# Kernel tuning notes

Measured on AMD Instinct MI355X. Metric: run time of the kernel, lower is better.

Reference implementation:

```python
import jax, jax.numpy as jnp
import numpy as np
import math

SIZE = (60, 270, 480)           # full video T, H, W
CHANNELS = 14                   # sum of per-level grid channels 8+4+2
GRID_SIZES = [(60, 16, 16, 8), (30, 8, 8, 4), (15, 4, 4, 2)]
IDX_MAX = (60, 3, 5)            # patch grid -> patch_size (1, 90, 96)
PADDING = (0, 1, 1)
N_PATCH = 64
MANIP_LBASE = 2.0
MANIP_LEVELS = 8
INIT_SCALE = 1e-3


def setup_inputs() -> dict:
    key = jax.random.key(0)
    kt, kh, kw = jax.random.split(key, 3)
    idx = jnp.stack([
        jax.random.randint(kt, (N_PATCH,), 0, IDX_MAX[0]),
        jax.random.randint(kh, (N_PATCH,), 0, IDX_MAX[1]),
        jax.random.randint(kw, (N_PATCH,), 0, IDX_MAX[2]),
    ], axis=1).astype(jnp.int32)
    inp = {
        "idx": idx,
        "idx_max": jnp.asarray(IDX_MAX, dtype=jnp.int32),
        "padding": jnp.asarray(PADDING, dtype=jnp.int32),
    }
    for i, (T, H, W, C) in enumerate(GRID_SIZES):
        k = jax.random.fold_in(key, 10 + i)
        inp[f"grid{i}"] = jax.random.normal(k, (T * H * W, C), jnp.float32) * INIT_SCALE
    return inp


def _pixel_idx_1d(ix, size_d, nmax_d, pad_d):
    # ix: [N] patch index along one dim -> ([N, P+2*pad] clipped pixel idx, mask)
    p = size_d // nmax_d
    offs = jnp.arange(-pad_d, p + pad_d)
    raw = ix[:, None] * p + offs[None, :]
    mask = ((raw >= 0) & (raw < size_d)).astype(jnp.float32)
    return jnp.clip(raw, 0, size_d - 1), mask


def reference(idx, idx_max, padding, grid0, grid1, grid2):
    T, H, W = SIZE
    im = tuple(int(v) for v in np.asarray(idx_max))
    pad = tuple(int(v) for v in np.asarray(padding))
    patch = tuple(SIZE[d] // im[d] for d in range(3))
    ppad = tuple(patch[d] + 2 * pad[d] for d in range(3))

    # Multi-level grids -> trilinear upsample to full (T,H,W,C_i), concat on C.
    # jax.image.resize 'trilinear' uses half-pixel centers == torch align_corners=False.
    enc_splits = []
    for g, (Tg, Hg, Wg, Cg) in zip((grid0, grid1, grid2), GRID_SIZES):
        enc_splits.append(jax.image.resize(g.reshape(Tg, Hg, Wg, Cg), (T, H, W, Cg), method="trilinear"))
    enc = jnp.concatenate(enc_splits, axis=-1).reshape(T * H * W, CHANNELS)

    it, mt = _pixel_idx_1d(idx[:, 0], T, im[0], pad[0])
    ih, mh = _pixel_idx_1d(idx[:, 1], H, im[1], pad[1])
    iw, mw = _pixel_idx_1d(idx[:, 2], W, im[2], pad[2])

    flat = (it[:, :, None, None] * (H * W) + ih[:, None, :, None] * W + iw[:, None, None, :]).reshape(-1)
    mask = (mt[:, :, None, None] * mh[:, None, :, None] * mw[:, None, None, :]).reshape(-1, 1)

    t_embed = (mask * enc[flat]).reshape((idx.shape[0],) + ppad + (CHANNELS,))

    bases = (MANIP_LBASE ** jnp.arange(MANIP_LEVELS, dtype=jnp.float32)) * math.pi
    v = idx[:, 0].astype(jnp.float32)[:, None] * bases
    t_manip = jnp.concatenate([jnp.sin(v), jnp.cos(v)], axis=-1)  # [N, 2*levels]

    return t_embed, t_manip
```

## Files before the change

kernel.cpp:

```cpp
#include <hip/hip_runtime.h>
#include <math.h>


#define N_PATCH 64
#define PPAD_H 92
#define PPAD_W 98
#define CH 14
#define PIX_PER_PATCH (PPAD_H * PPAD_W)
#define ROWS_PER_BLOCK 2
#define BLOCKS_PER_PATCH 46
#define PX_PER_BLOCK 196
#define F4_PER_BLOCK (PX_PER_BLOCK * CH / 4)
#define ELEMS_PER_PATCH (PIX_PER_PATCH * CH)
#define ELEMS_PER_BLOCK (PX_PER_BLOCK * CH)
#define TOTAL_EMBED (N_PATCH * ELEMS_PER_PATCH)
#define TOTAL_MANIP (N_PATCH * 16)

#define RB_STRIDE 72
#define L1_OFF 48
#define L2_OFF 64
#define BD_L1 40
#define BD_L2 52
#define BD_COUNT 56
#define BD_STRIDE 64

#define SW0 ((float)((double)16 / 480.0))
#define SW1 ((float)((double)8  / 480.0))
#define SW2 ((float)((double)4  / 480.0))
#define SH0 ((float)((double)16 / 270.0))
#define SH1 ((float)((double)8  / 270.0))
#define SH2 ((float)((double)4  / 270.0))

__device__ __forceinline__ float lerpf(float a, float b, float f) {
    return a + f * (b - a);
}

__device__ __forceinline__ int wcell0u(int rw0, float sw) {
    float x = ((float)rw0 + 0.5f) * sw - 0.5f;
    return (int)floorf(x);
}

__global__ __launch_bounds__(256) void embed_kernel(
    const int* __restrict__ idx,
    const float* __restrict__ g0,
    const float* __restrict__ g1,
    const float* __restrict__ g2,
    float* __restrict__ out)
{
    __shared__ __align__(16) float s_V[ROWS_PER_BLOCK][RB_STRIDE];
    __shared__ __align__(16) float s_B[ROWS_PER_BLOCK][BD_STRIDE];
    __shared__ __align__(16) float s_D[ROWS_PER_BLOCK][BD_STRIDE];
    __shared__ __align__(16) float s_buf[PX_PER_BLOCK * CH];

    const int tid = threadIdx.x;
    const int bx  = blockIdx.x;
    const int n   = blockIdx.y;
    const int it  = idx[3 * n + 0];
    const int ih  = idx[3 * n + 1];
    const int iw  = idx[3 * n + 2];
    const int rw0 = iw * 96 - 1;

    const int C0u0 = wcell0u(rw0, SW0);
    const int C0u1 = wcell0u(rw0, SW1);
    const int C0u2 = wcell0u(rw0, SW2);
    const int C0_0 = min(max(C0u0, 0), 15);
    const int C0_1 = min(max(C0u1, 0), 7);
    const int C0_2 = min(max(C0u2, 0), 3);

    if (bx == 0 && n == 0) {
        float* om = out + TOTAL_EMBED;
        for (int e = tid; e < TOTAL_MANIP; e += 256) {
            int nn = e >> 4;
            int j  = e & 15;
            int l  = j & 7;
            float base = (float)M_PI * (float)(1 << l);
            float v = (float)idx[3 * nn + 0] * base;
            double dv = (double)v;
            om[e] = (float)((j < 8) ? sin(dv) : cos(dv));
        }
    }

    if (tid < 96) {
        int chn  = tid & 7;
        int u    = tid >> 3;
        int row  = (u >= 6);
        int cell = u - 6 * row;
        int rh   = ih * 90 + (bx * 2 + row) - 1;
        float mh = ((unsigned)rh < 270u) ? 1.0f : 0.0f;
        float xh = ((float)rh + 0.5f) * SH0 - 0.5f;
        float ff = floorf(xh);
        float fh = xh - ff;
        int h0 = (int)ff;
        int h0c = min(max(h0, 0), 15), h1c = min(h0 + 1, 15);
        int cw = min(C0_0 + cell, 15);
        const float* base = g0 + (size_t)it * 2048;
        float a = base[(h0c * 16 + cw) * 8 + chn];
        float b = base[(h1c * 16 + cw) * 8 + chn];
        s_V[row][cell * 8 + chn] = mh * lerpf(a, b, fh);
    } else if (tid < 128) {
        int i    = tid - 96;
        int chn  = i & 3;
        int u    = i >> 2;
        int row  = (u >= 4);
        int cell = u - 4 * row;
        int rh   = ih * 90 + (bx * 2 + row) - 1;
        float mh = ((unsigned)rh < 270u) ? 1.0f : 0.0f;
        float xh = ((float)rh + 0.5f) * SH1 - 0.5f;
        float ff = floorf(xh);
        float fh = xh - ff;
        int h0 = (int)ff;
        int h0c = min(max(h0, 0), 7), h1c = min(h0 + 1, 7);
        float xt = ((float)it + 0.5f) * 0.5f - 0.5f;
        float ftf = floorf(xt);
        float ft  = xt - ftf;
        int t0 = (int)ftf;
        int t0c = min(max(t0, 0), 29), t1c = min(t0 + 1, 29);
        int cw = min(C0_1 + cell, 7);
        float a00 = g1[((t0c * 8 + h0c) * 8 + cw) * 4 + chn];
        float a01 = g1[((t0c * 8 + h1c) * 8 + cw) * 4 + chn];
        float a10 = g1[((t1c * 8 + h0c) * 8 + cw) * 4 + chn];
        float a11 = g1[((t1c * 8 + h1c) * 8 + cw) * 4 + chn];
        s_V[row][L1_OFF + cell * 4 + chn] =
            mh * lerpf(lerpf(a00, a01, fh), lerpf(a10, a11, fh), ft);
    } else if (tid < 140) {
        int i    = tid - 128;
        int chn  = i & 1;
        int u    = i >> 1;
        int row  = (u >= 3);
        int cell = u - 3 * row;
        int rh   = ih * 90 + (bx * 2 + row) - 1;
        float mh = ((unsigned)rh < 270u) ? 1.0f : 0.0f;
        float xh = ((float)rh + 0.5f) * SH2 - 0.5f;
        float ff = floorf(xh);
        float fh = xh - ff;
        int h0 = (int)ff;
        int h0c = min(max(h0, 0), 3), h1c = min(h0 + 1, 3);
        float xt = ((float)it + 0.5f) * 0.25f - 0.5f;
        float ftf = floorf(xt);
        float ft  = xt - ftf;
        int t0 = (int)ftf;
        int t0c = min(max(t0, 0), 14), t1c = min(t0 + 1, 14);
        int cw = min(C0_2 + cell, 3);
        float a00 = g2[((t0c * 4 + h0c) * 4 + cw) * 2 + chn];
        float a01 = g2[((t0c * 4 + h1c) * 4 + cw) * 2 + chn];
        float a10 = g2[((t1c * 4 + h0c) * 4 + cw) * 2 + chn];
        float a11 = g2[((t1c * 4 + h1c) * 4 + cw) * 2 + chn];
        s_V[row][L2_OFF + cell * 2 + chn] =
            mh * lerpf(lerpf(a00, a01, fh), lerpf(a10, a11, fh), ft);
    }
    __syncthreads();

    if (tid < 2 * 2 * BD_COUNT) {
        int row = tid >= 2 * BD_COUNT;
        int o   = tid - 2 * BD_COUNT * row;
        int d   = o >= BD_COUNT;
        int k   = o - BD_COUNT * d;
        int lvl, s0, chn, cs, vb, C0u, C0c, Wg1;
        if (k < BD_L1)      { lvl = 0; s0 = k >> 3; chn = k & 7;
                              cs = 8; vb = 0;      C0u = C0u0; C0c = C0_0; Wg1 = 15; }
        else if (k < BD_L2) { int kk = k - BD_L1; lvl = 1; s0 = kk >> 2; chn = kk & 3;
                              cs = 4; vb = L1_OFF; C0u = C0u1; C0c = C0_1; Wg1 = 7; }
        else                { int kk = k - BD_L2; lvl = 2; s0 = kk >> 1; chn = kk & 1;
                              cs = 2; vb = L2_OFF; C0u = C0u2; C0c = C0_2; Wg1 = 3; }
        (void)lvl;
        int w0 = C0u + s0;
        int wa = min(max(w0, 0), Wg1);
        int wb = min(w0 + 1, Wg1);
        float va = s_V[row][vb + (wa - C0c) * cs + chn];
        float vbv = s_V[row][vb + (wb - C0c) * cs + chn];
        if (d == 0) s_B[row][k] = va;
        else        s_D[row][k] = vbv - va;
    }
    __syncthreads();

    if (tid < PX_PER_BLOCK) {
        int row = (tid >= PPAD_W);
        int ww  = tid - PPAD_W * row;
        int rw  = iw * 96 + ww - 1;
        float2* b = (float2*)(s_buf + tid * CH);

        if (rw == -1 || rw == 480) {
            float2 z = make_float2(0.f, 0.f);
            b[0] = z; b[1] = z; b[2] = z; b[3] = z; b[4] = z; b[5] = z; b[6] = z;
        } else {
            float rwc = (float)rw + 0.5f;

            float x0 = rwc * SW0 - 0.5f;
            float f0f = floorf(x0);
            float fw0 = x0 - f0f;
            int s00 = (int)f0f - C0u0;
            float x1 = rwc * SW1 - 0.5f;
            float f1f = floorf(x1);
            float fw1 = x1 - f1f;
            int s01 = (int)f1f - C0u1;
            float x2 = rwc * SW2 - 0.5f;
            float f2f = floorf(x2);
            float fw2 = x2 - f2f;
            int s02 = (int)f2f - C0u2;

            const float* B = s_B[row];
            const float* D = s_D[row];
            float4 B0 = *(const float4*)(B + s00 * 8);
            float4 B1 = *(const float4*)(B + s00 * 8 + 4);
            float4 D0 = *(const float4*)(D + s00 * 8);
            float4 D1 = *(const float4*)(D + s00 * 8 + 4);
            float4 Bc = *(const float4*)(B + BD_L1 + s01 * 4);
            float4 Dc = *(const float4*)(D + BD_L1 + s01 * 4);
            float2 Be = *(const float2*)(B + BD_L2 + s02 * 2);
            float2 De = *(const float2*)(D + BD_L2 + s02 * 2);

            b[0] = make_float2(fmaf(fw0, D0.x, B0.x), fmaf(fw0, D0.y, B0.y));
            b[1] = make_float2(fmaf(fw0, D0.z, B0.z), fmaf(fw0, D0.w, B0.w));
            b[2] = make_float2(fmaf(fw0, D1.x, B1.x), fmaf(fw0, D1.y, B1.y));
            b[3] = make_float2(fmaf(fw0, D1.z, B1.z), fmaf(fw0, D1.w, B1.w));
            b[4] = make_float2(fmaf(fw1, Dc.x, Bc.x), fmaf(fw1, Dc.y, Bc.y));
            b[5] = make_float2(fmaf(fw1, Dc.z, Bc.z), fmaf(fw1, Dc.w, Bc.w));
            b[6] = make_float2(fmaf(fw2, De.x, Be.x), fmaf(fw2, De.y, Be.y));
        }
    }
    __syncthreads();

    const float4* sb = (const float4*)s_buf;
    float4* gb = (float4*)(out + (size_t)n * ELEMS_PER_PATCH + bx * ELEMS_PER_BLOCK);
    gb[tid]       = sb[tid];
    gb[tid + 256] = sb[tid + 256];
    if (tid < F4_PER_BLOCK - 512) gb[tid + 512] = sb[tid + 512];
}

extern "C" void kernel_launch(void* const* d_in, const int* in_sizes, int n_in,
                              void* d_out, int out_size, void* d_ws, size_t ws_size,
                              hipStream_t stream) {
    const int*   idx = (const int*)  d_in[0];
    const float* g0  = (const float*)d_in[3];
    const float* g1  = (const float*)d_in[4];
    const float* g2  = (const float*)d_in[5];
    float* out = (float*)d_out;

    dim3 grid(BLOCKS_PER_PATCH, N_PATCH);
    embed_kernel<<<grid, 256, 0, stream>>>(idx, g0, g1, g2, out);
}
```

Baseline: 15.40 us.

## Compute output float4s directly from interleaved B/D table, drop LDS staging buffer

The per-pixel interpolation stage no longer writes into a shared-memory staging buffer that is then copied out. Each thread now computes its coalesced float4 output chunks directly, working out which pixel, level and channel pair it covers. The B and D tables are interleaved into float4 units so one LDS read serves a channel pair. This removes a barrier and the shared-memory round trip, but adds per-element index arithmetic, divides and level-select branches.

```diff
diff --git a/kernel.cpp b/kernel.cpp
--- a/kernel.cpp
+++ b/kernel.cpp
@@ -9,20 +9,17 @@
 #define PIX_PER_PATCH (PPAD_H * PPAD_W)
 #define ROWS_PER_BLOCK 2
 #define BLOCKS_PER_PATCH 46
-#define PX_PER_BLOCK 196
-#define F4_PER_BLOCK (PX_PER_BLOCK * CH / 4)
+#define F4_PER_ROW (PPAD_W * CH / 4)
+#define F4_PER_BLOCK (2 * F4_PER_ROW)
 #define ELEMS_PER_PATCH (PIX_PER_PATCH * CH)
-#define ELEMS_PER_BLOCK (PX_PER_BLOCK * CH)
+#define ELEMS_PER_BLOCK (2 * PPAD_W * CH)
 #define TOTAL_EMBED (N_PATCH * ELEMS_PER_PATCH)
 #define TOTAL_MANIP (N_PATCH * 16)
 
 #define RB_STRIDE 72
 #define L1_OFF 48
 #define L2_OFF 64
-#define BD_L1 40
-#define BD_L2 52
-#define BD_COUNT 56
-#define BD_STRIDE 64
+#define BD_UNITS 28
 
 #define SW0 ((float)((double)16 / 480.0))
 #define SW1 ((float)((double)8  / 480.0))
@@ -47,10 +44,8 @@
     const float* __restrict__ g2,
     float* __restrict__ out)
 {
-    __shared__ __align__(16) float s_V[ROWS_PER_BLOCK][RB_STRIDE];
-    __shared__ __align__(16) float s_B[ROWS_PER_BLOCK][BD_STRIDE];
-    __shared__ __align__(16) float s_D[ROWS_PER_BLOCK][BD_STRIDE];
-    __shared__ __align__(16) float s_buf[PX_PER_BLOCK * CH];
+    __shared__ __align__(16) float  s_V[ROWS_PER_BLOCK][RB_STRIDE];
+    __shared__ __align__(16) float4 s_BD[ROWS_PER_BLOCK][BD_UNITS];
 
     const int tid = threadIdx.x;
     const int bx  = blockIdx.x;
@@ -150,81 +145,59 @@
     }
     __syncthreads();
 
-    if (tid < 2 * 2 * BD_COUNT) {
-        int row = tid >= 2 * BD_COUNT;
-        int o   = tid - 2 * BD_COUNT * row;
-        int d   = o >= BD_COUNT;
-        int k   = o - BD_COUNT * d;
-        int lvl, s0, chn, cs, vb, C0u, C0c, Wg1;
-        if (k < BD_L1)      { lvl = 0; s0 = k >> 3; chn = k & 7;
-                              cs = 8; vb = 0;      C0u = C0u0; C0c = C0_0; Wg1 = 15; }
-        else if (k < BD_L2) { int kk = k - BD_L1; lvl = 1; s0 = kk >> 2; chn = kk & 3;
-                              cs = 4; vb = L1_OFF; C0u = C0u1; C0c = C0_1; Wg1 = 7; }
-        else                { int kk = k - BD_L2; lvl = 2; s0 = kk >> 1; chn = kk & 1;
-                              cs = 2; vb = L2_OFF; C0u = C0u2; C0c = C0_2; Wg1 = 3; }
-        (void)lvl;
+    if (tid < 224) {
+        int row = tid >= 112;
+        int o   = tid - 112 * row;
+        int u   = o >> 2;
+        int c   = o & 3;
+        int s0, cs, vb, C0u, C0c, Wg1, ch;
+        if (u < 20)      { s0 = u >> 2;        cs = 8; vb = 0;      C0u = C0u0; C0c = C0_0; Wg1 = 15; ch = 2 * (u & 3); }
+        else if (u < 26) { int uu = u - 20; s0 = uu >> 1; cs = 4; vb = L1_OFF; C0u = C0u1; C0c = C0_1; Wg1 = 7;  ch = 2 * (uu & 1); }
+        else             { s0 = u - 26;        cs = 2; vb = L2_OFF; C0u = C0u2; C0c = C0_2; Wg1 = 3;  ch = 0; }
         int w0 = C0u + s0;
         int wa = min(max(w0, 0), Wg1);
         int wb = min(w0 + 1, Wg1);
-        float va = s_V[row][vb + (wa - C0c) * cs + chn];
-        float vbv = s_V[row][vb + (wb - C0c) * cs + chn];
-        if (d == 0) s_B[row][k] = va;
-        else        s_D[row][k] = vbv - va;
+        int cc = c & 1;
+        float va  = s_V[row][vb + (wa - C0c) * cs + ch + cc];
+        float vbv = s_V[row][vb + (wb - C0c) * cs + ch + cc];
+        ((float*)&s_BD[row][u])[c] = (c < 2) ? va : (vbv - va);
     }
     __syncthreads();
 
-    if (tid < PX_PER_BLOCK) {
-        int row = (tid >= PPAD_W);
-        int ww  = tid - PPAD_W * row;
-        int rw  = iw * 96 + ww - 1;
-        float2* b = (float2*)(s_buf + tid * CH);
-
-        if (rw == -1 || rw == 480) {
-            float2 z = make_float2(0.f, 0.f);
-            b[0] = z; b[1] = z; b[2] = z; b[3] = z; b[4] = z; b[5] = z; b[6] = z;
-        } else {
-            float rwc = (float)rw + 0.5f;
-
-            float x0 = rwc * SW0 - 0.5f;
-            float f0f = floorf(x0);
-            float fw0 = x0 - f0f;
-            int s00 = (int)f0f - C0u0;
-            float x1 = rwc * SW1 - 0.5f;
-            float f1f = floorf(x1);
-            float fw1 = x1 - f1f;
-            int s01 = (int)f1f - C0u1;
-            float x2 = rwc * SW2 - 0.5f;
-            float f2f = floorf(x2);
-            float fw2 = x2 - f2f;
-            int s02 = (int)f2f - C0u2;
-
-            const float* B = s_B[row];
-            const float* D = s_D[row];
-            float4 B0 = *(const float4*)(B + s00 * 8);
-            float4 B1 = *(const float4*)(B + s00 * 8 + 4);
-            float4 D0 = *(const float4*)(D + s00 * 8);
-            float4 D1 = *(const float4*)(D + s00 * 8 + 4);
-            float4 Bc = *(const float4*)(B + BD_L1 + s01 * 4);
-            float4 Dc = *(const float4*)(D + BD_L1 + s01 * 4);
-            float2 Be = *(const float2*)(B + BD_L2 + s02 * 2);
-            float2 De = *(const float2*)(D + BD_L2 + s02 * 2);
-
-            b[0] = make_float2(fmaf(fw0, D0.x, B0.x), fmaf(fw0, D0.y, B0.y));
-            b[1] = make_float2(fmaf(fw0, D0.z, B0.z), fmaf(fw0, D0.w, B0.w));
-            b[2] = make_float2(fmaf(fw0, D1.x, B1.x), fmaf(fw0, D1.y, B1.y));
-            b[3] = make_float2(fmaf(fw0, D1.z, B1.z), fmaf(fw0, D1.w, B1.w));
-            b[4] = make_float2(fmaf(fw1, Dc.x, Bc.x), fmaf(fw1, Dc.y, Bc.y));
-            b[5] = make_float2(fmaf(fw1, Dc.z, Bc.z), fmaf(fw1, Dc.w, Bc.w));
-            b[6] = make_float2(fmaf(fw2, De.x, Be.x), fmaf(fw2, De.y, Be.y));
-        }
-    }
-    __syncthreads();
-
-    const float4* sb = (const float4*)s_buf;
     float4* gb = (float4*)(out + (size_t)n * ELEMS_PER_PATCH + bx * ELEMS_PER_BLOCK);
-    gb[tid]       = sb[tid];
-    gb[tid + 256] = sb[tid + 256];
-    if (tid < F4_PER_BLOCK - 512) gb[tid + 512] = sb[tid + 512];
+
+    auto pairval = [&](int P, int row, float& rx, float& ry) {
+        int p = P / 7;
+        int q = P - 7 * p;
+        int rw = iw * 96 + p - 1;
+        float mw = ((unsigned)rw < 480u) ? 1.0f : 0.0f;
+        float rwc = (float)rw + 0.5f;
+        int lvl = (q >= 4) + (q >= 6);
+        float sw  = (lvl == 0) ? SW0 : ((lvl == 1) ? SW1 : SW2);
+        int   C0u = (lvl == 0) ? C0u0 : ((lvl == 1) ? C0u1 : C0u2);
+        float x  = rwc * sw - 0.5f;
+        float ffl = floorf(x);
+        float fw = x - ffl;
+        int s0 = (int)ffl - C0u;
+        int unit = (lvl == 0) ? (s0 * 4 + q)
+                 : ((lvl == 1) ? (20 + s0 * 2 + (q - 4)) : (26 + s0));
+        float4 bd = s_BD[row][unit];
+        rx = mw * fmaf(fw, bd.z, bd.x);
+        ry = mw * fmaf(fw, bd.w, bd.y);
+    };
+
+    auto do_f4 = [&](int j) {
+        int row = j >= F4_PER_ROW;
+        int P0  = 2 * (j - F4_PER_ROW * row);
+        float r0x, r0y, r1x, r1y;
+        pairval(P0,     row, r0x, r0y);
+        pairval(P0 + 1, row, r1x, r1y);
+        gb[j] = make_float4(r0x, r0y, r1x, r1y);
+    };
+
+    do_f4(tid);
+    do_f4(tid + 256);
+    if (tid < F4_PER_BLOCK - 512) do_f4(tid + 512);
 }
 
 extern "C" void kernel_launch(void* const* d_in, const int* in_sizes, int n_in,
```

Result: slower. 28.98 us (+88.2%).
